# Kernel tuning notes

Hardware: AMD Instinct MI355X
Metric: run time of the kernel (lower is better)

## Reference

```python
import jax, jax.numpy as jnp
import numpy as np

B, T, D, H = 4, 2048, 1024, 16
DK = D // H  # 64


def setup_inputs() -> dict:
    key = jax.random.key(0)
    ks = jax.random.split(key, 8)
    std = 1.0 / np.sqrt(2.0 * D)  # initialize_weights: normal(0, 1/sqrt(2*d_model*(i_layer+1))), i_layer=0
    inp = {
        "q": jax.random.normal(ks[0], (B, T, D), jnp.float32),
        "k": jax.random.normal(ks[1], (B, T, D), jnp.float32),
        "v": jax.random.normal(ks[2], (B, T, D), jnp.float32),
        "Wq": jax.random.normal(ks[3], (D, D), jnp.float32) * std,
        "Wk": jax.random.normal(ks[4], (D, D), jnp.float32) * std,
        "Wv": jax.random.normal(ks[5], (D, D), jnp.float32) * std,
        "Wo": jax.random.normal(ks[6], (D, D), jnp.float32) * std,
        "bq": jnp.zeros((D,), jnp.float32),
        "bk": jnp.zeros((D,), jnp.float32),
        "bv": jnp.zeros((D,), jnp.float32),
        "bo": jnp.zeros((D,), jnp.float32),
    }
    return inp


def _split_heads(x):
    # (B,T,D) -> (B,H,T,DK), same as x.view(B,T,H,DK).transpose(1,2)
    b, t, _ = x.shape
    return x.reshape(b, t, H, DK).transpose(0, 2, 1, 3)


def reference(q, k, v, Wq, Wk, Wv, Wo, bq, bk, bv, bo):
    # Linear projections (torch Linear: x @ W.T + b)
    qh = _split_heads(q @ Wq.T + bq)  # (B,H,T,DK)
    kh = _split_heads(k @ Wk.T + bk)
    vh = _split_heads(v @ Wv.T + bv)

    # scaled dot-product similarities: (B,H,Tq,Tk)
    scores = jnp.einsum("bhqd,bhkd->bhqk", qh, kh) / jnp.sqrt(jnp.float32(DK))

    # causal mask: tril(ones)==0 positions filled with -inf
    tq, tk = scores.shape[-2], scores.shape[-1]
    causal = jnp.tril(jnp.ones((tq, tk), dtype=bool))
    scores = jnp.where(causal, scores, jnp.float32(-jnp.inf))

    attn = jax.nn.softmax(scores, axis=-1)  # (B,H,Tq,Tk)
    ctx = jnp.einsum("bhqk,bhkd->bhqd", attn, vh)  # (B,H,Tq,DK)

    # merge heads: (B,H,T,DK) -> (B,T,D), then output projection
    merged = ctx.transpose(0, 2, 1, 3).reshape(q.shape[0], tq, D)
    return merged @ Wo.T + bo
```

## Files before the change

kernel.cpp:

```cpp
#include <hip/hip_runtime.h>
#include <hip/hip_bf16.h>
#include <stdint.h>

#define B_ 4
#define T_ 2048
#define D_ 1024
#define H_ 16
#define DK_ 64
#define M_ (B_*T_)

typedef __attribute__((ext_vector_type(8))) short bf16x8;
typedef __attribute__((ext_vector_type(4))) short bf16x4;
typedef __attribute__((ext_vector_type(4))) float f32x4;
typedef __hip_bfloat16 bf16;

__device__ __forceinline__ void gld_lds16(const bf16* g, bf16* l) {
  __builtin_amdgcn_global_load_lds((const __attribute__((address_space(1))) void*)g,
                                   (__attribute__((address_space(3))) void*)l,
                                   16, 0, 0);
}

__device__ __forceinline__ short bfbits(float f) {
  union { bf16 h; short s; } u; u.h = __float2bfloat16(f); return u.s;
}

__global__ __launch_bounds__(256) void cvt_all(
    const float* __restrict__ q, const float* __restrict__ k, const float* __restrict__ v,
    const float* __restrict__ wq, const float* __restrict__ wk,
    const float* __restrict__ wv, const float* __restrict__ wo,
    bf16* __restrict__ qb, bf16* __restrict__ kb, bf16* __restrict__ vb,
    bf16* __restrict__ wqb, bf16* __restrict__ wkb,
    bf16* __restrict__ wvb, bf16* __restrict__ wob) {
  int gid = blockIdx.x * 256 + threadIdx.x;
  const float* src; bf16* dst; int off;
  if (gid < 6291456) {
    int s = gid >> 21; off = gid & 2097151;
    src = (s == 0) ? q : (s == 1) ? k : v;
    dst = (s == 0) ? qb : (s == 1) ? kb : vb;
  } else {
    int g2 = gid - 6291456;
    int s = g2 >> 18; off = g2 & 262143;
    src = (s == 0) ? wq : (s == 1) ? wk : (s == 2) ? wv : wo;
    dst = (s == 0) ? wqb : (s == 1) ? wkb : (s == 2) ? wvb : wob;
  }
  float4 val = reinterpret_cast<const float4*>(src)[off];
  union { ushort4 u; bf16 h[4]; } o;
  o.h[0] = __float2bfloat16(val.x);
  o.h[1] = __float2bfloat16(val.y);
  o.h[2] = __float2bfloat16(val.z);
  o.h[3] = __float2bfloat16(val.w);
  reinterpret_cast<ushort4*>(dst)[off] = o.u;
}

__global__ __launch_bounds__(512) void proj_qkv(
    const bf16* __restrict__ qb, const bf16* __restrict__ kb, const bf16* __restrict__ vb,
    const bf16* __restrict__ Wqb, const bf16* __restrict__ Wkb, const bf16* __restrict__ Wvb,
    const float* __restrict__ bq, const float* __restrict__ bk, const float* __restrict__ bv,
    bf16* __restrict__ Qh, bf16* __restrict__ Kh, bf16* __restrict__ Vt) {
  constexpr int K = 1024;
  constexpr int BK = 64;
  __shared__ __align__(16) bf16 As[256 * BK];
  __shared__ __align__(16) bf16 Bs[128 * BK];

  const int z = blockIdx.z;
  const bool vt = (z == 2);
  const bf16* A  = (z == 0) ? qb : (z == 1) ? kb : Wvb;
  const bf16* Bm = (z == 0) ? Wqb : (z == 1) ? Wkb : vb;
  const float* bias = (z == 0) ? bq : (z == 1) ? bk : bv;
  bf16* out = (z == 0) ? Qh : (z == 1) ? Kh : Vt;
  const float scale = (z == 0) ? 0.125f * 1.4426950408889634f : 1.0f;

  int bm, bn;
  if (vt) { int flat = blockIdx.x + 32 * blockIdx.y; bm = flat >> 6; bn = flat & 63; }
  else    { bm = blockIdx.x; bn = blockIdx.y; }

  const int tid = threadIdx.x;
  const int w = tid >> 6, l = tid & 63;
  const int wm = w >> 1, wn = w & 1;
  const int lr = l & 15, lk = l >> 4;

  f32x4 acc[4][4] = {};

  for (int k0 = 0; k0 < K; k0 += BK) {
#pragma unroll
    for (int i = 0; i < 4; ++i) {
      int p = i * 512 + tid;
      int row = p >> 3;
      int so = (p & 7) ^ (row & 7);
      gld_lds16(A + (size_t)(bm * 256 + row) * K + k0 + so * 8, &As[p * 8]);
    }
#pragma unroll
    for (int i = 0; i < 2; ++i) {
      int p = i * 512 + tid;
      int row = p >> 3;
      int so = (p & 7) ^ (row & 7);
      gld_lds16(Bm + (size_t)(bn * 128 + row) * K + k0 + so * 8, &Bs[p * 8]);
    }
    __syncthreads();

#pragma unroll
    for (int kk = 0; kk < 2; ++kk) {
      bf16x8 af[4], bfr[4];
#pragma unroll
      for (int m = 0; m < 4; ++m) {
        int row = wm * 64 + m * 16 + lr;
        int slot = (kk * 4 + lk) ^ (row & 7);
        af[m] = *reinterpret_cast<const bf16x8*>(&As[row * BK + slot * 8]);
      }
#pragma unroll
      for (int n = 0; n < 4; ++n) {
        int row = wn * 64 + n * 16 + lr;
        int slot = (kk * 4 + lk) ^ (row & 7);
        bfr[n] = *reinterpret_cast<const bf16x8*>(&Bs[row * BK + slot * 8]);
      }
#pragma unroll
      for (int m = 0; m < 4; ++m)
#pragma unroll
        for (int n = 0; n < 4; ++n)
          acc[m][n] = __builtin_amdgcn_mfma_f32_16x16x32_bf16(af[m], bfr[n], acc[m][n], 0, 0, 0);
    }
    __syncthreads();
  }

  const int crow0 = bm * 256 + wm * 64;
  const int ccol0 = bn * 128 + wn * 64;
#pragma unroll
  for (int m = 0; m < 4; ++m) {
#pragma unroll
    for (int n = 0; n < 4; ++n) {
#pragma unroll
      for (int r = 0; r < 4; ++r) {
        const int row = crow0 + m * 16 + lk * 4 + r;
        const int col = ccol0 + n * 16 + lr;
        if (!vt) {
          float vv = (acc[m][n][r] + bias[col]) * scale;
          size_t idx = (((size_t)(row >> 11) * H_ + (col >> 6)) * T_ + (row & (T_ - 1))) * DK_ + (col & (DK_ - 1));
          out[idx] = __float2bfloat16(vv);
        } else {
          float vv = acc[m][n][r] + bias[row];
          size_t idx = (size_t)(col >> 11) * ((size_t)H_ * DK_ * T_) + (size_t)row * T_ + (col & (T_ - 1));
          out[idx] = __float2bfloat16(vv);
        }
      }
    }
  }
}

__global__ __launch_bounds__(512) void gemm_out(const bf16* __restrict__ A,
                                                const bf16* __restrict__ Bm,
                                                const float* __restrict__ bias,
                                                float* __restrict__ Cout) {
  constexpr int K = 1024;
  constexpr int BK = 64;
  __shared__ __align__(16) bf16 As[256 * BK];
  __shared__ __align__(16) bf16 Bs[128 * BK];

  const int bm = blockIdx.x;
  const int bn = blockIdx.y;
  const int tid = threadIdx.x;
  const int w = tid >> 6, l = tid & 63;
  const int wm = w >> 1, wn = w & 1;
  const int lr = l & 15, lk = l >> 4;

  f32x4 acc[4][4] = {};

  for (int k0 = 0; k0 < K; k0 += BK) {
#pragma unroll
    for (int i = 0; i < 4; ++i) {
      int p = i * 512 + tid;
      int row = p >> 3;
      int so = (p & 7) ^ (row & 7);
      gld_lds16(A + (size_t)(bm * 256 + row) * K + k0 + so * 8, &As[p * 8]);
    }
#pragma unroll
    for (int i = 0; i < 2; ++i) {
      int p = i * 512 + tid;
      int row = p >> 3;
      int so = (p & 7) ^ (row & 7);
      gld_lds16(Bm + (size_t)(bn * 128 + row) * K + k0 + so * 8, &Bs[p * 8]);
    }
    __syncthreads();

#pragma unroll
    for (int kk = 0; kk < 2; ++kk) {
      bf16x8 af[4], bfr[4];
#pragma unroll
      for (int m = 0; m < 4; ++m) {
        int row = wm * 64 + m * 16 + lr;
        int slot = (kk * 4 + lk) ^ (row & 7);
        af[m] = *reinterpret_cast<const bf16x8*>(&As[row * BK + slot * 8]);
      }
#pragma unroll
      for (int n = 0; n < 4; ++n) {
        int row = wn * 64 + n * 16 + lr;
        int slot = (kk * 4 + lk) ^ (row & 7);
        bfr[n] = *reinterpret_cast<const bf16x8*>(&Bs[row * BK + slot * 8]);
      }
#pragma unroll
      for (int m = 0; m < 4; ++m)
#pragma unroll
        for (int n = 0; n < 4; ++n)
          acc[m][n] = __builtin_amdgcn_mfma_f32_16x16x32_bf16(af[m], bfr[n], acc[m][n], 0, 0, 0);
    }
    __syncthreads();
  }

  const int crow0 = bm * 256 + wm * 64;
  const int ccol0 = bn * 128 + wn * 64;
#pragma unroll
  for (int m = 0; m < 4; ++m) {
#pragma unroll
    for (int n = 0; n < 4; ++n) {
#pragma unroll
      for (int r = 0; r < 4; ++r) {
        const int row = crow0 + m * 16 + lk * 4 + r;
        const int col = ccol0 + n * 16 + lr;
        Cout[(size_t)row * D_ + col] = acc[m][n][r] + bias[col];
      }
    }
  }
}

__global__ __launch_bounds__(256, 7) void attn_fwd(const bf16* __restrict__ Qh,
                                                   const bf16* __restrict__ Kh,
                                                   const bf16* __restrict__ Vt,
                                                   bf16* __restrict__ ctx) {
  __shared__ __align__(16) bf16 Kbuf[2][32 * 64];
  __shared__ __align__(16) bf16 Vbuf[2][32 * 64];
  __shared__ __align__(16) char Ps[4][16 * 80];

  const int tid = threadIdx.x, w = tid >> 6, l = tid & 63;
  const int lr = l & 15, lk = l >> 4;
  const int bid = blockIdx.x;
  const int head = bid & 63;
  const int t = 31 - (bid >> 6);
  char* Pw = &Ps[w][0];

  const bf16* Qb = Qh + (size_t)head * T_ * DK_;
  const bf16* Kb = Kh + (size_t)head * T_ * DK_;
  const bf16* Vb = Vt + (size_t)head * DK_ * T_;
  const int bb = head >> 4, hh = head & 15;

  const int r0 = t * 64;
  const int nt32 = 2 * (t + 1);
  const int qrow = r0 + w * 16 + lr;
  const int jd = (r0 + w * 16) >> 5;

  const bf16* qp = Qb + (size_t)qrow * DK_ + lk * 8;
  bf16x8 qf0 = *reinterpret_cast<const bf16x8*>(qp);
  bf16x8 qf1 = *reinterpret_cast<const bf16x8*>(qp + 32);

  f32x4 oacc[4] = {};
  float srow = 0.f;

  {
    int p = tid;
    int krow = p >> 3;
    int kso = (p & 7) ^ (krow & 7);
    gld_lds16(Kb + (size_t)krow * DK_ + kso * 8, &Kbuf[0][p * 8]);
    int vrow = p >> 3;
    int u = (p & 7) ^ (vrow & 7);
    int dk = vrow * 2 + (u >> 2);
    gld_lds16(Vb + (size_t)dk * T_ + (u & 3) * 8, &Vbuf[0][p * 8]);
  }
  __syncthreads();

  int buf = 0;
#pragma unroll 1
  for (int j = 0; j < nt32; ++j) {
    if (j + 1 < nt32) {
      const int k0n = (j + 1) * 32;
      int p = tid;
      int krow = p >> 3;
      int kso = (p & 7) ^ (krow & 7);
      gld_lds16(Kb + (size_t)(k0n + krow) * DK_ + kso * 8, &Kbuf[buf ^ 1][p * 8]);
      int vrow = p >> 3;
      int u = (p & 7) ^ (vrow & 7);
      int dk = vrow * 2 + (u >> 2);
      gld_lds16(Vb + (size_t)dk * T_ + k0n + (u & 3) * 8, &Vbuf[buf ^ 1][p * 8]);
    }

    if (j <= jd) {
      f32x4 sacc[2] = {};
      __builtin_amdgcn_s_setprio(1);
#pragma unroll
      for (int n = 0; n < 2; ++n) {
        int row = n * 16 + lr;
        int s0 = lk ^ (row & 7);
        int s1 = (4 + lk) ^ (row & 7);
        bf16x8 kf0 = *reinterpret_cast<const bf16x8*>(&Kbuf[buf][row * 64 + s0 * 8]);
        bf16x8 kf1 = *reinterpret_cast<const bf16x8*>(&Kbuf[buf][row * 64 + s1 * 8]);
        sacc[n] = __builtin_amdgcn_mfma_f32_16x16x32_bf16(kf0, qf0, sacc[n], 0, 0, 0);
        sacc[n] = __builtin_amdgcn_mfma_f32_16x16x32_bf16(kf1, qf1, sacc[n], 0, 0, 0);
      }
      __builtin_amdgcn_s_setprio(0);

      if (j == jd) {
#pragma unroll
        for (int n = 0; n < 2; ++n)
#pragma unroll
          for (int r = 0; r < 4; ++r)
            if (j * 32 + n * 16 + lk * 4 + r > qrow) sacc[n][r] = -1e30f;
      }

      float ts = 0.f;
#pragma unroll
      for (int n = 0; n < 2; ++n) {
        float p0 = __builtin_exp2f(sacc[n][0]);
        float p1 = __builtin_exp2f(sacc[n][1]);
        float p2 = __builtin_exp2f(sacc[n][2]);
        float p3 = __builtin_exp2f(sacc[n][3]);
        ts += (p0 + p1) + (p2 + p3);
        bf16x4 pk;
        pk[0] = bfbits(p0); pk[1] = bfbits(p1); pk[2] = bfbits(p2); pk[3] = bfbits(p3);
        *reinterpret_cast<bf16x4*>(Pw + lr * 80 + n * 32 + lk * 8) = pk;
      }
      ts += __shfl_xor(ts, 16, 64);
      ts += __shfl_xor(ts, 32, 64);
      srow += ts;

      bf16x8 pa = *reinterpret_cast<const bf16x8*>(Pw + lr * 80 + lk * 16);

      __builtin_amdgcn_s_setprio(1);
#pragma unroll
      for (int n = 0; n < 4; ++n) {
        int rowp = n * 8 + (lr >> 1);
        int u = (lr & 1) * 4 + lk;
        int s = u ^ (rowp & 7);
        bf16x8 vf = *reinterpret_cast<const bf16x8*>(&Vbuf[buf][rowp * 64 + s * 8]);
        oacc[n] = __builtin_amdgcn_mfma_f32_16x16x32_bf16(vf, pa, oacc[n], 0, 0, 0);
      }
      __builtin_amdgcn_s_setprio(0);
    }

    __syncthreads();
    buf ^= 1;
  }

  const float inv = 1.0f / srow;
#pragma unroll
  for (int n = 0; n < 4; ++n) {
    bf16x4 pk;
#pragma unroll
    for (int r = 0; r < 4; ++r) pk[r] = bfbits(oacc[n][r] * inv);
    *reinterpret_cast<bf16x4*>(&ctx[((size_t)(bb * T_ + qrow)) * D_ + hh * DK_ + n * 16 + lk * 4]) = pk;
  }
}

extern "C" void kernel_launch(void* const* d_in, const int* in_sizes, int n_in,
                              void* d_out, int out_size, void* d_ws, size_t ws_size,
                              hipStream_t stream) {
  const float* q  = (const float*)d_in[0];
  const float* k  = (const float*)d_in[1];
  const float* v  = (const float*)d_in[2];
  const float* Wq = (const float*)d_in[3];
  const float* Wk = (const float*)d_in[4];
  const float* Wv = (const float*)d_in[5];
  const float* Wo = (const float*)d_in[6];
  const float* bq = (const float*)d_in[7];
  const float* bk = (const float*)d_in[8];
  const float* bv = (const float*)d_in[9];
  const float* bo = (const float*)d_in[10];

  constexpr size_t E_IN = (size_t)M_ * D_;
  constexpr size_t E_W  = (size_t)D_ * D_;
  char* ws = (char*)d_ws;
  size_t off = 0;
  bf16* qb  = (bf16*)(ws + off); off += E_IN * 2;
  bf16* kb  = (bf16*)(ws + off); off += E_IN * 2;
  bf16* vb  = (bf16*)(ws + off); off += E_IN * 2;
  bf16* Wqb = (bf16*)(ws + off); off += E_W * 2;
  bf16* Wkb = (bf16*)(ws + off); off += E_W * 2;
  bf16* Wvb = (bf16*)(ws + off); off += E_W * 2;
  bf16* Wob = (bf16*)(ws + off); off += E_W * 2;
  bf16* Qh  = (bf16*)(ws + off); off += E_IN * 2;
  bf16* Kh  = (bf16*)(ws + off); off += E_IN * 2;
  bf16* Vtw = (bf16*)(ws + off); off += E_IN * 2;
  bf16* ctx = (bf16*)(ws + off); off += E_IN * 2;

  cvt_all<<<dim3(28672), dim3(256), 0, stream>>>(q, k, v, Wq, Wk, Wv, Wo,
                                                 qb, kb, vb, Wqb, Wkb, Wvb, Wob);

  proj_qkv<<<dim3(32, 8, 3), dim3(512), 0, stream>>>(qb, kb, vb, Wqb, Wkb, Wvb,
                                                     bq, bk, bv, Qh, Kh, Vtw);

  attn_fwd<<<dim3(2048), dim3(256), 0, stream>>>(Qh, Kh, Vtw, ctx);

  gemm_out<<<dim3(32, 8), dim3(512), 0, stream>>>(ctx, Wob, bo, (float*)d_out);
}
```

Measured before the change: 191.8 us.

## Triple-buffer QKV projection GEMM with interleaved async loads and MFMA

Restructures the proj_qkv main loop into a three-stage LDS ring buffer. Tiles are prefetched two steps ahead with global_load_lds, and the A/B staging is split into four chunks interleaved between per-row MFMA groups. Hand-placed s_waitcnt and s_barrier calls replace the per-iteration __syncthreads, and s_setprio raises priority around the MFMA bursts. The aim is to hide global-memory latency behind matrix math, at the cost of roughly 1.5x the LDS footprint (occupancy) and fragile manual vmcnt bookkeeping.

After: 256.4 us. +33.7%, slower.

```diff
diff --git a/kernel.cpp b/kernel.cpp
--- a/kernel.cpp
+++ b/kernel.cpp
@@ -59,8 +59,9 @@
     bf16* __restrict__ Qh, bf16* __restrict__ Kh, bf16* __restrict__ Vt) {
   constexpr int K = 1024;
   constexpr int BK = 64;
-  __shared__ __align__(16) bf16 As[256 * BK];
-  __shared__ __align__(16) bf16 Bs[128 * BK];
+  constexpr int NT = 16;
+  __shared__ __align__(16) bf16 As[3][2][128 * 64];
+  __shared__ __align__(16) bf16 Bs[3][128 * 64];
 
   const int z = blockIdx.z;
   const bool vt = (z == 2);
@@ -80,46 +81,81 @@
   const int lr = l & 15, lk = l >> 4;
 
   f32x4 acc[4][4] = {};
-
-  for (int k0 = 0; k0 < K; k0 += BK) {
-#pragma unroll
-    for (int i = 0; i < 4; ++i) {
-      int p = i * 512 + tid;
-      int row = p >> 3;
-      int so = (p & 7) ^ (row & 7);
-      gld_lds16(A + (size_t)(bm * 256 + row) * K + k0 + so * 8, &As[p * 8]);
-    }
+  bf16x8 bfrag[4][2];
+
+  auto stgA = [&](int t2, int sl, int h) {
 #pragma unroll
     for (int i = 0; i < 2; ++i) {
       int p = i * 512 + tid;
       int row = p >> 3;
       int so = (p & 7) ^ (row & 7);
-      gld_lds16(Bm + (size_t)(bn * 128 + row) * K + k0 + so * 8, &Bs[p * 8]);
-    }
-    __syncthreads();
-
-#pragma unroll
-    for (int kk = 0; kk < 2; ++kk) {
-      bf16x8 af[4], bfr[4];
-#pragma unroll
-      for (int m = 0; m < 4; ++m) {
-        int row = wm * 64 + m * 16 + lr;
-        int slot = (kk * 4 + lk) ^ (row & 7);
-        af[m] = *reinterpret_cast<const bf16x8*>(&As[row * BK + slot * 8]);
-      }
-#pragma unroll
-      for (int n = 0; n < 4; ++n) {
-        int row = wn * 64 + n * 16 + lr;
-        int slot = (kk * 4 + lk) ^ (row & 7);
-        bfr[n] = *reinterpret_cast<const bf16x8*>(&Bs[row * BK + slot * 8]);
-      }
-#pragma unroll
-      for (int m = 0; m < 4; ++m)
-#pragma unroll
-        for (int n = 0; n < 4; ++n)
-          acc[m][n] = __builtin_amdgcn_mfma_f32_16x16x32_bf16(af[m], bfr[n], acc[m][n], 0, 0, 0);
-    }
-    __syncthreads();
+      gld_lds16(A + (size_t)(bm * 256 + h * 128 + row) * K + t2 * BK + so * 8,
+                &As[sl][h][p * 8]);
+    }
+  };
+  auto stgB = [&](int t2, int sl, int part) {
+    int p = part * 512 + tid;
+    int row = p >> 3;
+    int so = (p & 7) ^ (row & 7);
+    gld_lds16(Bm + (size_t)(bn * 128 + row) * K + t2 * BK + so * 8,
+              &Bs[sl][p * 8]);
+  };
+
+  stgA(0, 0, 0); stgA(0, 0, 1); stgB(0, 0, 0); stgB(0, 0, 1);
+  stgA(1, 1, 0); stgA(1, 1, 1); stgB(1, 1, 0); stgB(1, 1, 1);
+  asm volatile("s_waitcnt vmcnt(6)" ::: "memory");
+  asm volatile("s_barrier" ::: "memory");
+
+  int sl0 = 0;
+#pragma unroll 1
+  for (int t = 0; t < NT; ++t) {
+    const int sl2 = (sl0 + 2 >= 3) ? sl0 - 1 : sl0 + 2;
+    const bool pre = (t + 2 < NT);
+
+    auto mfma_row = [&](int m) {
+      int lrow = (wm & 1) * 64 + m * 16 + lr;
+      int a0s = lk ^ (lrow & 7);
+      int a1s = (4 + lk) ^ (lrow & 7);
+      bf16x8 a0 = *reinterpret_cast<const bf16x8*>(&As[sl0][wm >> 1][lrow * 64 + a0s * 8]);
+      bf16x8 a1 = *reinterpret_cast<const bf16x8*>(&As[sl0][wm >> 1][lrow * 64 + a1s * 8]);
+      asm volatile("s_barrier" ::: "memory");
+      __builtin_amdgcn_s_setprio(1);
+#pragma unroll
+      for (int n = 0; n < 4; ++n)
+        acc[m][n] = __builtin_amdgcn_mfma_f32_16x16x32_bf16(a0, bfrag[n][0], acc[m][n], 0, 0, 0);
+#pragma unroll
+      for (int n = 0; n < 4; ++n)
+        acc[m][n] = __builtin_amdgcn_mfma_f32_16x16x32_bf16(a1, bfrag[n][1], acc[m][n], 0, 0, 0);
+      __builtin_amdgcn_s_setprio(0);
+    };
+
+    if (pre) stgA(t + 2, sl2, 0);
+#pragma unroll
+    for (int n = 0; n < 4; ++n) {
+      int brow = wn * 64 + n * 16 + lr;
+      int b0s = lk ^ (brow & 7);
+      int b1s = (4 + lk) ^ (brow & 7);
+      bfrag[n][0] = *reinterpret_cast<const bf16x8*>(&Bs[sl0][brow * 64 + b0s * 8]);
+      bfrag[n][1] = *reinterpret_cast<const bf16x8*>(&Bs[sl0][brow * 64 + b1s * 8]);
+    }
+    mfma_row(0);
+    asm volatile("s_barrier" ::: "memory");
+
+    if (pre) stgA(t + 2, sl2, 1);
+    mfma_row(1);
+    asm volatile("s_barrier" ::: "memory");
+
+    if (pre) stgB(t + 2, sl2, 0);
+    mfma_row(2);
+    asm volatile("s_barrier" ::: "memory");
+
+    if (pre) stgB(t + 2, sl2, 1);
+    mfma_row(3);
+    if (t + 3 < NT) asm volatile("s_waitcnt vmcnt(6)" ::: "memory");
+    else            asm volatile("s_waitcnt vmcnt(0)" ::: "memory");
+    asm volatile("s_barrier" ::: "memory");
+
+    sl0 = (sl0 + 1 >= 3) ? 0 : sl0 + 1;
   }
 
   const int crow0 = bm * 256 + wm * 64;
```

## Double-buffer projection GEMM LDS tiles with BK=32 and prefetch next tile

Applied to the files above, without the earlier changes.

Both the QKV projection and output GEMM now use two LDS buffers with a K-step of 32, issuing global-to-LDS loads for the next tile before computing on the current one. This removes one barrier per iteration and overlaps memory traffic with MFMA work. The swizzle packs two rows per 64-element LDS row to keep reads conflict-free, and s_setprio raises priority around the MFMA block. The cost is twice as many loop iterations with fewer MFMAs each, and it relies on a single barrier per iteration to guard against buffer reuse hazards.

Result: slower. 203.9 us (+6.3%).

```diff
diff --git a/kernel.cpp b/kernel.cpp
--- a/kernel.cpp
+++ b/kernel.cpp
@@ -58,9 +58,10 @@
     const float* __restrict__ bq, const float* __restrict__ bk, const float* __restrict__ bv,
     bf16* __restrict__ Qh, bf16* __restrict__ Kh, bf16* __restrict__ Vt) {
   constexpr int K = 1024;
-  constexpr int BK = 64;
-  __shared__ __align__(16) bf16 As[256 * BK];
-  __shared__ __align__(16) bf16 Bs[128 * BK];
+  constexpr int BK = 32;
+  constexpr int NT = K / BK;
+  __shared__ __align__(16) bf16 As[2][128 * 64];
+  __shared__ __align__(16) bf16 Bs[2][64 * 64];
 
   const int z = blockIdx.z;
   const bool vt = (z == 2);
@@ -81,45 +82,58 @@
 
   f32x4 acc[4][4] = {};
 
-  for (int k0 = 0; k0 < K; k0 += BK) {
-#pragma unroll
-    for (int i = 0; i < 4; ++i) {
-      int p = i * 512 + tid;
-      int row = p >> 3;
-      int so = (p & 7) ^ (row & 7);
-      gld_lds16(A + (size_t)(bm * 256 + row) * K + k0 + so * 8, &As[p * 8]);
-    }
+  auto stgA = [&](int t, int b) {
 #pragma unroll
     for (int i = 0; i < 2; ++i) {
-      int p = i * 512 + tid;
-      int row = p >> 3;
-      int so = (p & 7) ^ (row & 7);
-      gld_lds16(Bm + (size_t)(bn * 128 + row) * K + k0 + so * 8, &Bs[p * 8]);
-    }
+      int p16 = i * 512 + tid;
+      int pr = p16 >> 3, s = p16 & 7;
+      int u = s ^ (pr & 7);
+      int grow = pr * 2 + (u >> 2);
+      gld_lds16(A + (size_t)(bm * 256 + grow) * K + t * BK + (u & 3) * 8,
+                &As[b][p16 * 8]);
+    }
+  };
+  auto stgB = [&](int t, int b) {
+    int p16 = tid;
+    int pr = p16 >> 3, s = p16 & 7;
+    int u = s ^ (pr & 7);
+    int grow = pr * 2 + (u >> 2);
+    gld_lds16(Bm + (size_t)(bn * 128 + grow) * K + t * BK + (u & 3) * 8,
+              &Bs[b][p16 * 8]);
+  };
+
+  stgA(0, 0); stgB(0, 0);
+
+#pragma unroll 1
+  for (int t = 0; t < NT; ++t) {
     __syncthreads();
-
-#pragma unroll
-    for (int kk = 0; kk < 2; ++kk) {
-      bf16x8 af[4], bfr[4];
-#pragma unroll
-      for (int m = 0; m < 4; ++m) {
-        int row = wm * 64 + m * 16 + lr;
-        int slot = (kk * 4 + lk) ^ (row & 7);
-        af[m] = *reinterpret_cast<const bf16x8*>(&As[row * BK + slot * 8]);
-      }
-#pragma unroll
-      for (int n = 0; n < 4; ++n) {
-        int row = wn * 64 + n * 16 + lr;
-        int slot = (kk * 4 + lk) ^ (row & 7);
-        bfr[n] = *reinterpret_cast<const bf16x8*>(&Bs[row * BK + slot * 8]);
-      }
-#pragma unroll
-      for (int m = 0; m < 4; ++m)
-#pragma unroll
-        for (int n = 0; n < 4; ++n)
-          acc[m][n] = __builtin_amdgcn_mfma_f32_16x16x32_bf16(af[m], bfr[n], acc[m][n], 0, 0, 0);
-    }
-    __syncthreads();
+    if (t + 1 < NT) { stgA(t + 1, (t + 1) & 1); stgB(t + 1, (t + 1) & 1); }
+
+    const int b = t & 1;
+    bf16x8 af[4], bfr[4];
+#pragma unroll
+    for (int m = 0; m < 4; ++m) {
+      int trow = wm * 64 + m * 16 + lr;
+      int pr = trow >> 1;
+      int u = (trow & 1) * 4 + lk;
+      int s = u ^ (pr & 7);
+      af[m] = *reinterpret_cast<const bf16x8*>(&As[b][(pr * 8 + s) * 8]);
+    }
+#pragma unroll
+    for (int n = 0; n < 4; ++n) {
+      int trow = wn * 64 + n * 16 + lr;
+      int pr = trow >> 1;
+      int u = (trow & 1) * 4 + lk;
+      int s = u ^ (pr & 7);
+      bfr[n] = *reinterpret_cast<const bf16x8*>(&Bs[b][(pr * 8 + s) * 8]);
+    }
+    __builtin_amdgcn_s_setprio(1);
+#pragma unroll
+    for (int m = 0; m < 4; ++m)
+#pragma unroll
+      for (int n = 0; n < 4; ++n)
+        acc[m][n] = __builtin_amdgcn_mfma_f32_16x16x32_bf16(af[m], bfr[n], acc[m][n], 0, 0, 0);
+    __builtin_amdgcn_s_setprio(0);
   }
 
   const int crow0 = bm * 256 + wm * 64;
@@ -151,9 +165,10 @@
                                                 const float* __restrict__ bias,
                                                 float* __restrict__ Cout) {
   constexpr int K = 1024;
-  constexpr int BK = 64;
-  __shared__ __align__(16) bf16 As[256 * BK];
-  __shared__ __align__(16) bf16 Bs[128 * BK];
+  constexpr int BK = 32;
+  constexpr int NT = K / BK;
+  __shared__ __align__(16) bf16 As[2][128 * 64];
+  __shared__ __align__(16) bf16 Bs[2][64 * 64];
 
   const int bm = blockIdx.x;
   const int bn = blockIdx.y;
@@ -164,45 +179,58 @@
 
   f32x4 acc[4][4] = {};
 
-  for (int k0 = 0; k0 < K; k0 += BK) {
-#pragma unroll
-    for (int i = 0; i < 4; ++i) {
-      int p = i * 512 + tid;
-      int row = p >> 3;
-      int so = (p & 7) ^ (row & 7);
-      gld_lds16(A + (size_t)(bm * 256 + row) * K + k0 + so * 8, &As[p * 8]);
-    }
+  auto stgA = [&](int t, int b) {
 #pragma unroll
     for (int i = 0; i < 2; ++i) {
-      int p = i * 512 + tid;
-      int row = p >> 3;
-      int so = (p & 7) ^ (row & 7);
-      gld_lds16(Bm + (size_t)(bn * 128 + row) * K + k0 + so * 8, &Bs[p * 8]);
-    }
+      int p16 = i * 512 + tid;
+      int pr = p16 >> 3, s = p16 & 7;
+      int u = s ^ (pr & 7);
+      int grow = pr * 2 + (u >> 2);
+      gld_lds16(A + (size_t)(bm * 256 + grow) * K + t * BK + (u & 3) * 8,
+                &As[b][p16 * 8]);
+    }
+  };
+  auto stgB = [&](int t, int b) {
+    int p16 = tid;
+    int pr = p16 >> 3, s = p16 & 7;
+    int u = s ^ (pr & 7);
+    int grow = pr * 2 + (u >> 2);
+    gld_lds16(Bm + (size_t)(bn * 128 + grow) * K + t * BK + (u & 3) * 8,
+              &Bs[b][p16 * 8]);
+  };
+
+  stgA(0, 0); stgB(0, 0);
+
+#pragma unroll 1
+  for (int t = 0; t < NT; ++t) {
     __syncthreads();
-
-#pragma unroll
-    for (int kk = 0; kk < 2; ++kk) {
-      bf16x8 af[4], bfr[4];
-#pragma unroll
-      for (int m = 0; m < 4; ++m) {
-        int row = wm * 64 + m * 16 + lr;
-        int slot = (kk * 4 + lk) ^ (row & 7);
-        af[m] = *reinterpret_cast<const bf16x8*>(&As[row * BK + slot * 8]);
-      }
-#pragma unroll
-      for (int n = 0; n < 4; ++n) {
-        int row = wn * 64 + n * 16 + lr;
-        int slot = (kk * 4 + lk) ^ (row & 7);
-        bfr[n] = *reinterpret_cast<const bf16x8*>(&Bs[row * BK + slot * 8]);
-      }
-#pragma unroll
-      for (int m = 0; m < 4; ++m)
-#pragma unroll
-        for (int n = 0; n < 4; ++n)
-          acc[m][n] = __builtin_amdgcn_mfma_f32_16x16x32_bf16(af[m], bfr[n], acc[m][n], 0, 0, 0);
-    }
-    __syncthreads();
+    if (t + 1 < NT) { stgA(t + 1, (t + 1) & 1); stgB(t + 1, (t + 1) & 1); }
+
+    const int b = t & 1;
+    bf16x8 af[4], bfr[4];
+#pragma unroll
+    for (int m = 0; m < 4; ++m) {
+      int trow = wm * 64 + m * 16 + lr;
+      int pr = trow >> 1;
+      int u = (trow & 1) * 4 + lk;
+      int s = u ^ (pr & 7);
+      af[m] = *reinterpret_cast<const bf16x8*>(&As[b][(pr * 8 + s) * 8]);
+    }
+#pragma unroll
+    for (int n = 0; n < 4; ++n) {
+      int trow = wn * 64 + n * 16 + lr;
+      int pr = trow >> 1;
+      int u = (trow & 1) * 4 + lk;
+      int s = u ^ (pr & 7);
+      bfr[n] = *reinterpret_cast<const bf16x8*>(&Bs[b][(pr * 8 + s) * 8]);
+    }
+    __builtin_amdgcn_s_setprio(1);
+#pragma unroll
+    for (int m = 0; m < 4; ++m)
+#pragma unroll
+      for (int n = 0; n < 4; ++n)
+        acc[m][n] = __builtin_amdgcn_mfma_f32_16x16x32_bf16(af[m], bfr[n], acc[m][n], 0, 0, 0);
+    __builtin_amdgcn_s_setprio(0);
   }
 
   const int crow0 = bm * 256 + wm * 64;
```
